# Kernel tuning notes

Measured on AMD Instinct MI355X. Metric: run time of the kernel, lower is better.

Reference implementation:

```python
import jax, jax.numpy as jnp
import numpy as np

B, L, N, C, H, COND = 2, 8, 256, 1024, 16, 64
D = C // H  # 64, divisible by 4


def setup_inputs() -> dict:
    key = jax.random.key(0)
    ks = jax.random.split(key, 16)
    w = lambda k, i, o: (jax.random.normal(k, (i, o), jnp.float32) / np.sqrt(i)).astype(jnp.float32)
    return {
        "s_frames": jax.random.normal(ks[0], (B, L, N, C), jnp.float32),
        "frame_idx": jnp.arange(L, dtype=jnp.int32),
        "seq_idx": jnp.sort(jax.random.randint(ks[1], (B, N), 0, 1024), axis=-1).astype(jnp.int32),
        "mask": jax.random.randint(ks[2], (B, L, N), 0, 2).astype(jnp.int32),
        "cond": jax.random.normal(ks[3], (B, COND), jnp.float32),
        "W_ada": w(ks[4], COND, 2 * C), "b_ada": jnp.zeros((2 * C,), jnp.float32),
        "Wq": w(ks[5], C, C), "bq": jnp.zeros((C,), jnp.float32),
        "Wk": w(ks[6], C, C), "bk": jnp.zeros((C,), jnp.float32),
        "Wv": w(ks[7], C, C), "bv": jnp.zeros((C,), jnp.float32),
        "Wo": w(ks[8], C, C), "bo": jnp.zeros((C,), jnp.float32),
    }


def _rope2d(x, pos_s, pos_f, inv_freq):
    # x: [B,H,T,D]; first half of D rotated by residue positions, second half by frame positions.
    half = x.shape[-1] // 2
    quarter = half // 2

    def rot(xh, pos):  # xh [B,H,T,half], pos [B,T]
        ang = pos[:, None, :, None] * inv_freq  # [B,1,T,quarter]
        c, s = jnp.cos(ang), jnp.sin(ang)
        x1, x2 = xh[..., :quarter], xh[..., quarter:]
        return jnp.concatenate([x1 * c - x2 * s, x1 * s + x2 * c], axis=-1)

    return jnp.concatenate([rot(x[..., :half], pos_s), rot(x[..., half:], pos_f)], axis=-1)


def reference(s_frames, frame_idx, seq_idx, mask, cond,
              W_ada, b_ada, Wq, bq, Wk, bk, Wv, bv, Wo, bo):
    Bx, Lx, Nx, Cx = s_frames.shape
    T = Lx * Nx
    Dh = Cx // H
    scale = Dh ** (-0.5)

    # AdaLN: LayerNorm (no affine) then conditional scale/shift from cond
    mu = s_frames.mean(-1, keepdims=True)
    var = ((s_frames - mu) ** 2).mean(-1, keepdims=True)
    xn = (s_frames - mu) * jax.lax.rsqrt(var + 1e-5)
    ss = cond @ W_ada + b_ada                      # [B, 2C]
    shift, sc = ss[:, :Cx], ss[:, Cx:]
    x = xn * (1.0 + sc[:, None, None, :]) + shift[:, None, None, :]

    xf = x.reshape(Bx, T, Cx)
    split = lambda t: t.reshape(Bx, T, H, Dh).transpose(0, 2, 1, 3)  # [B,H,T,D]
    q = split(xf @ Wq + bq)
    k = split(xf @ Wk + bk)
    v = split(xf @ Wv + bv)

    # 2D RoPE positions (token t = l*N + n)
    half = Dh // 2
    quarter = half // 2
    inv_freq = 1.0 / (10000.0 ** (jnp.arange(quarter, dtype=jnp.float32) * 2.0 / half))
    pos_s = jnp.tile(seq_idx, (1, Lx)).astype(jnp.float32)                                  # [B,T]
    pos_f = jnp.broadcast_to(jnp.repeat(frame_idx, Nx).astype(jnp.float32)[None], (Bx, T))  # [B,T]
    q = _rope2d(q, pos_s, pos_f, inv_freq)
    k = _rope2d(k, pos_s, pos_f, inv_freq)

    # additive bias: block-causal over frames + key padding mask
    fi = jnp.repeat(jnp.arange(Lx), Nx)                      # [T]
    future = fi[None, :] > fi[:, None]                       # [T,T] key frame > query frame
    bias = jnp.where(future, -jnp.inf, 0.0)[None, None]      # [1,1,T,T]
    pad = (mask.reshape(Bx, T) == 0)
    bias = jnp.where(pad[:, None, None, :], -jnp.inf, bias)  # [B,1,T,T]

    logits = jnp.einsum('bhtd,bhsd->bhts', q, k) * scale + bias
    w = jax.nn.softmax(logits, axis=-1)
    out = jnp.einsum('bhts,bhsd->bhtd', w, v)
    out = out.transpose(0, 2, 1, 3).reshape(Bx, Lx, Nx, Cx)
    return out @ Wo + bo
```

## Files before the change

### kernel.cpp

```cpp
#include <hip/hip_runtime.h>

typedef __bf16 bf16;
typedef __bf16 bf16x8 __attribute__((ext_vector_type(8)));
typedef __bf16 bf16x4 __attribute__((ext_vector_type(4)));
typedef float  f32x4  __attribute__((ext_vector_type(4)));

#define B_ 2
#define L_ 8
#define N_ 256
#define C_ 1024
#define H_ 16
#define D_ 64
#define T_ 2048
#define M_ 4096
#define COND_ 64

#define QSCALE 0.18033688011111372f

__device__ __forceinline__ void gload_lds16(const void* g, void* lds) {
  __builtin_amdgcn_global_load_lds((const __attribute__((address_space(1))) void*)g,
                                   (__attribute__((address_space(3))) void*)lds, 16, 0, 0);
}

__global__ __launch_bounds__(256) void k_ada(const float* __restrict__ cond,
                                             const float* __restrict__ W,
                                             const float* __restrict__ ba,
                                             float* __restrict__ ss) {
  int j = blockIdx.x * 256 + threadIdx.x;
  int b = j >> 11;
  int n = j & 2047;
  float s = ba[n];
  #pragma unroll
  for (int i = 0; i < COND_; ++i) s += cond[b * COND_ + i] * W[i * 2048 + n];
  ss[j] = s;
}

__global__ __launch_bounds__(256) void k_wt(const float* __restrict__ Wq,
                                            const float* __restrict__ Wk,
                                            const float* __restrict__ Wv,
                                            const float* __restrict__ Wo,
                                            bf16* __restrict__ Wt) {
  __shared__ float lds[64][65];
  int z = blockIdx.z;
  const float* W = (z == 0) ? Wq : (z == 1) ? Wk : (z == 2) ? Wv : Wo;
  int k0 = blockIdx.y * 64, n0 = blockIdx.x * 64;
  int tid = threadIdx.x;
  int r = tid >> 4, c4 = (tid & 15) * 4;
  #pragma unroll
  for (int p = 0; p < 4; ++p) {
    float4 v = *(const float4*)&W[(size_t)(k0 + p * 16 + r) * 1024 + n0 + c4];
    lds[p * 16 + r][c4] = v.x; lds[p * 16 + r][c4 + 1] = v.y;
    lds[p * 16 + r][c4 + 2] = v.z; lds[p * 16 + r][c4 + 3] = v.w;
  }
  __syncthreads();
  #pragma unroll
  for (int p = 0; p < 4; ++p) {
    int j = p * 16 + r;
    int i0 = c4;
    bf16x4 o;
    o[0] = (bf16)lds[i0][j]; o[1] = (bf16)lds[i0 + 1][j];
    o[2] = (bf16)lds[i0 + 2][j]; o[3] = (bf16)lds[i0 + 3][j];
    *(bf16x4*)&Wt[(size_t)(z * 1024 + n0 + j) * 1024 + k0 + i0] = o;
  }
}

__global__ __launch_bounds__(256) void k_ln(const float* __restrict__ x,
                                            const float* __restrict__ ss,
                                            bf16* __restrict__ xo) {
  int row = blockIdx.x;
  int b = row >> 11;
  int tid = threadIdx.x;
  float4 v = *(const float4*)&x[(size_t)row * 1024 + tid * 4];
  float s = v.x + v.y + v.z + v.w;
  float s2 = v.x * v.x + v.y * v.y + v.z * v.z + v.w * v.w;
  #pragma unroll
  for (int o = 32; o > 0; o >>= 1) { s += __shfl_down(s, o); s2 += __shfl_down(s2, o); }
  __shared__ float rs[4], rs2[4];
  int w = tid >> 6, l = tid & 63;
  if (l == 0) { rs[w] = s; rs2[w] = s2; }
  __syncthreads();
  s = rs[0] + rs[1] + rs[2] + rs[3];
  s2 = rs2[0] + rs2[1] + rs2[2] + rs2[3];
  float mu = s * (1.f / 1024.f);
  float var = s2 * (1.f / 1024.f) - mu * mu;
  float rinv = rsqrtf(var + 1e-5f);
  int c = tid * 4;
  float4 sh = *(const float4*)&ss[b * 2048 + c];
  float4 sc = *(const float4*)&ss[b * 2048 + 1024 + c];
  bf16x4 o;
  o[0] = (bf16)((v.x - mu) * rinv * (1.f + sc.x) + sh.x);
  o[1] = (bf16)((v.y - mu) * rinv * (1.f + sc.y) + sh.y);
  o[2] = (bf16)((v.z - mu) * rinv * (1.f + sc.z) + sh.z);
  o[3] = (bf16)((v.w - mu) * rinv * (1.f + sc.w) + sh.w);
  *(bf16x4*)&xo[(size_t)row * 1024 + c] = o;
}

__global__ __launch_bounds__(256) void k_gemm_qkv(const bf16* __restrict__ A,
                                                  const bf16* __restrict__ Bt,
                                                  const float* __restrict__ bq,
                                                  const float* __restrict__ bk,
                                                  const float* __restrict__ bv,
                                                  const int* __restrict__ seq_idx,
                                                  const int* __restrict__ frame_idx,
                                                  bf16* __restrict__ qkv,
                                                  bf16* __restrict__ vt) {
  __shared__ __attribute__((aligned(16))) bf16 As[3][64 * 32];
  __shared__ __attribute__((aligned(16))) bf16 Bs[3][128 * 32];
  const int K = 1024;
  int n0 = blockIdx.x * 128, m0 = blockIdx.y * 64;
  int tid = threadIdx.x;
  int w = tid >> 6, l = tid & 63, cc = l & 15, g = l >> 4;
  int wm = w >> 1, wn = w & 1;
  f32x4 acc[2][4] = {};
  int pxg = ((tid & 3) ^ ((tid >> 3) & 3)) * 8;
  const bf16* Ag = A + (size_t)(m0 + (tid >> 2)) * K + pxg;
  const bf16* Bg = Bt + (size_t)(n0 + (tid >> 2)) * K + pxg;
  int soff = w * 512;
  #define GSTAGE(buf, kt_)                                                      \
    do {                                                                        \
      gload_lds16(Ag + (kt_) * 32, &As[buf][soff]);                             \
      gload_lds16(Bg + (kt_) * 32, &Bs[buf][soff]);                             \
      gload_lds16(Bg + (kt_) * 32 + (size_t)64 * K, &Bs[buf][soff + 2048]);     \
    } while (0)
  GSTAGE(0, 0);
  GSTAGE(1, 1);
  int c0 = 0, c1 = 1, c2 = 2;
  int swz = (g ^ ((cc >> 1) & 3)) * 8;
  for (int kt = 0; kt < 32; ++kt) {
    if (kt + 2 < 32) {
      GSTAGE(c2, kt + 2);
      asm volatile("s_waitcnt vmcnt(6)" ::: "memory");
    } else if (kt + 1 < 32) {
      asm volatile("s_waitcnt vmcnt(3)" ::: "memory");
    } else {
      asm volatile("s_waitcnt vmcnt(0)" ::: "memory");
    }
    __builtin_amdgcn_s_barrier();
    asm volatile("" ::: "memory");
    bf16x8 a[2], bb[4];
    #pragma unroll
    for (int mi = 0; mi < 2; ++mi) a[mi] = *(const bf16x8*)&As[c0][(wm * 32 + mi * 16 + cc) * 32 + swz];
    #pragma unroll
    for (int ni = 0; ni < 4; ++ni) bb[ni] = *(const bf16x8*)&Bs[c0][(wn * 64 + ni * 16 + cc) * 32 + swz];
    #pragma unroll
    for (int mi = 0; mi < 2; ++mi)
      #pragma unroll
      for (int ni = 0; ni < 4; ++ni)
        acc[mi][ni] = __builtin_amdgcn_mfma_f32_16x16x32_bf16(a[mi], bb[ni], acc[mi][ni], 0, 0, 0);
    __builtin_amdgcn_s_barrier();
    asm volatile("" ::: "memory");
    int tmp = c0; c0 = c1; c1 = c2; c2 = tmp;
  }
  #undef GSTAGE
  int region = blockIdx.x >> 3;
  const float* bp = (region == 0) ? bq : (region == 1) ? bk : bv;
  int b = m0 >> 11;
  if (region < 2) {
    float* Ps = (float*)&As[0][0];
    if (tid < 64) Ps[tid] = (float)seq_idx[b * 256 + (m0 & 255) + tid];
    __syncthreads();
    float invf = exp2f(-0.8304820237218405f * (float)cc);
    float posf = (float)frame_idx[(m0 & 2047) >> 8];
    float snf, csf;
    sincosf(posf * invf, &snf, &csf);
    float scl = (region == 0) ? QSCALE : 1.0f;
    csf *= scl; snf *= scl;
    int colbase = n0 + wn * 64 + cc;
    float b0 = bp[colbase & 1023];
    float b1 = bp[(colbase + 16) & 1023];
    float b2 = bp[(colbase + 32) & 1023];
    float b3 = bp[(colbase + 48) & 1023];
    #pragma unroll
    for (int mi = 0; mi < 2; ++mi) {
      #pragma unroll
      for (int r = 0; r < 4; ++r) {
        int lr = wm * 32 + mi * 16 + g * 4 + r;
        float sns, css;
        sincosf(Ps[lr] * invf, &sns, &css);
        css *= scl; sns *= scl;
        float x0 = acc[mi][0][r] + b0;
        float x1 = acc[mi][1][r] + b1;
        float x2 = acc[mi][2][r] + b2;
        float x3 = acc[mi][3][r] + b3;
        bf16* op = qkv + (size_t)(m0 + lr) * 3072 + colbase;
        op[0]  = (bf16)(x0 * css - x1 * sns);
        op[16] = (bf16)(x0 * sns + x1 * css);
        op[32] = (bf16)(x2 * csf - x3 * snf);
        op[48] = (bf16)(x2 * snf + x3 * csf);
      }
    }
  } else {
    int h = (blockIdx.x - 16) * 2 + wn;
    int tbase = (m0 & 2047) + wm * 32;
    #pragma unroll
    for (int ni = 0; ni < 4; ++ni) {
      int d = ni * 16 + cc;
      float bias = bp[h * 64 + d];
      #pragma unroll
      for (int mi = 0; mi < 2; ++mi) {
        bf16x4 pk;
        #pragma unroll
        for (int r = 0; r < 4; ++r) pk[r] = (bf16)(acc[mi][ni][r] + bias);
        int t = tbase + mi * 16 + g * 4;
        *(bf16x4*)&vt[((size_t)(b * 16 + h) * 64 + d) * 2048 + t] = pk;
      }
    }
  }
}

__global__ __launch_bounds__(256) void k_gemm_o(const bf16* __restrict__ A,
                                                const bf16* __restrict__ Bt,
                                                const float* __restrict__ bo,
                                                float* __restrict__ out) {
  __shared__ __attribute__((aligned(16))) bf16 As[3][64 * 32];
  __shared__ __attribute__((aligned(16))) bf16 Bs[3][128 * 32];
  const int K = 1024;
  int n0 = blockIdx.x * 128, m0 = blockIdx.y * 64;
  int tid = threadIdx.x;
  int w = tid >> 6, l = tid & 63, cc = l & 15, g = l >> 4;
  int wm = w >> 1, wn = w & 1;
  f32x4 acc[2][4] = {};
  int pxg = ((tid & 3) ^ ((tid >> 3) & 3)) * 8;
  const bf16* Ag = A + (size_t)(m0 + (tid >> 2)) * K + pxg;
  const bf16* Bg = Bt + (size_t)(n0 + (tid >> 2)) * K + pxg;
  int soff = w * 512;
  #define GSTAGE(buf, kt_)                                                      \
    do {                                                                        \
      gload_lds16(Ag + (kt_) * 32, &As[buf][soff]);                             \
      gload_lds16(Bg + (kt_) * 32, &Bs[buf][soff]);                             \
      gload_lds16(Bg + (kt_) * 32 + (size_t)64 * K, &Bs[buf][soff + 2048]);     \
    } while (0)
  GSTAGE(0, 0);
  GSTAGE(1, 1);
  int c0 = 0, c1 = 1, c2 = 2;
  int swz = (g ^ ((cc >> 1) & 3)) * 8;
  for (int kt = 0; kt < 32; ++kt) {
    if (kt + 2 < 32) {
      GSTAGE(c2, kt + 2);
      asm volatile("s_waitcnt vmcnt(6)" ::: "memory");
    } else if (kt + 1 < 32) {
      asm volatile("s_waitcnt vmcnt(3)" ::: "memory");
    } else {
      asm volatile("s_waitcnt vmcnt(0)" ::: "memory");
    }
    __builtin_amdgcn_s_barrier();
    asm volatile("" ::: "memory");
    bf16x8 a[2], bb[4];
    #pragma unroll
    for (int mi = 0; mi < 2; ++mi) a[mi] = *(const bf16x8*)&As[c0][(wm * 32 + mi * 16 + cc) * 32 + swz];
    #pragma unroll
    for (int ni = 0; ni < 4; ++ni) bb[ni] = *(const bf16x8*)&Bs[c0][(wn * 64 + ni * 16 + cc) * 32 + swz];
    #pragma unroll
    for (int mi = 0; mi < 2; ++mi)
      #pragma unroll
      for (int ni = 0; ni < 4; ++ni)
        acc[mi][ni] = __builtin_amdgcn_mfma_f32_16x16x32_bf16(a[mi], bb[ni], acc[mi][ni], 0, 0, 0);
    __builtin_amdgcn_s_barrier();
    asm volatile("" ::: "memory");
    int tmp = c0; c0 = c1; c1 = c2; c2 = tmp;
  }
  #undef GSTAGE
  #pragma unroll
  for (int ni = 0; ni < 4; ++ni) {
    int col = n0 + wn * 64 + ni * 16 + cc;
    float bias = bo[col];
    #pragma unroll
    for (int mi = 0; mi < 2; ++mi)
      #pragma unroll
      for (int r = 0; r < 4; ++r) {
        int row = m0 + wm * 32 + mi * 16 + g * 4 + r;
        out[(size_t)row * 1024 + col] = acc[mi][ni][r] + bias;
      }
  }
}

__global__ __launch_bounds__(256) void k_attn(const bf16* __restrict__ qkv,
                                              const bf16* __restrict__ vt,
                                              const int* __restrict__ mask,
                                              bf16* __restrict__ out) {
  __shared__ __attribute__((aligned(16))) bf16 Ks[2][64 * 64];
  __shared__ __attribute__((aligned(16))) bf16 Vs[2][64 * 64];
  __shared__ __attribute__((aligned(16))) bf16 Plds[4][16][72];
  __shared__ int Ms[2048];
  int wid = blockIdx.x;
  int f = 7 - (wid >> 7);
  int rem = wid & 127;
  int h = rem >> 3;
  int b = (rem >> 2) & 1;
  int tile = rem & 3;
  int t0 = f * 256 + tile * 64;
  int nchunk = (f + 1) * 4;
  int tid = threadIdx.x;
  int w = tid >> 6, l = tid & 63, cc = l & 15, g = l >> 4;

  int rbase = w * 16 + (l >> 3);
  int px = (l & 7) ^ (l >> 3);
  int ldst = w * 1024 + l * 8;

  int trow = t0 + w * 16 + cc;
  const bf16* qp = qkv + (size_t)((size_t)b * T_ + trow) * 3072 + h * 64;
  bf16x8 aq0 = *(const bf16x8*)(qp + g * 8);
  bf16x8 aq1 = *(const bf16x8*)(qp + 32 + g * 8);
  f32x4 o[4] = {};
  f32x4 o1 = {0.f, 0.f, 0.f, 0.f};
  float mrow[4] = {-1e30f, -1e30f, -1e30f, -1e30f};
  const int* mp = mask + b * T_;

  bf16x8 onesv;
  #pragma unroll
  for (int u = 0; u < 8; ++u) onesv[u] = (bf16)1.0f;

  #pragma unroll
  for (int j = 0; j < 2; ++j)
    gload_lds16(mp + w * 512 + j * 256 + l * 4, &Ms[w * 512 + j * 256 + l * 4]);

  #define STAGE(buf, s0_)                                                              \
    do {                                                                               \
      _Pragma("unroll")                                                                \
      for (int j = 0; j < 2; ++j) {                                                    \
        int r_ = rbase + j * 8;                                                        \
        gload_lds16(qkv + (size_t)((size_t)b * T_ + (s0_) + r_) * 3072 + 1024 + h * 64 + px * 8, \
                    &Ks[buf][ldst + j * 512]);                                         \
        gload_lds16(vt + (size_t)((size_t)(b * H_ + h) * 64 + r_) * T_ + (s0_) + px * 8, \
                    &Vs[buf][ldst + j * 512]);                                         \
      }                                                                                \
    } while (0)

  STAGE(0, 0);
  int sw1 = (g ^ (cc & 7)) * 8;
  int sw2 = ((g + 4) ^ (cc & 7)) * 8;
  for (int scn = 0; scn < nchunk; ++scn) {
    int s0 = scn * 64;
    int cur = scn & 1;
    if (scn + 1 < nchunk) {
      STAGE(cur ^ 1, s0 + 64);
      asm volatile("s_waitcnt vmcnt(4)" ::: "memory");
    } else {
      asm volatile("s_waitcnt vmcnt(0)" ::: "memory");
    }
    __builtin_amdgcn_s_barrier();
    asm volatile("" ::: "memory");
    float biasv[4];
    #pragma unroll
    for (int ni = 0; ni < 4; ++ni) biasv[ni] = Ms[s0 + ni * 16 + cc] ? 0.f : -1e30f;
    f32x4 sac[4];
    #pragma unroll
    for (int ni = 0; ni < 4; ++ni) {
      int r = ni * 16 + cc;
      bf16x8 b0 = *(const bf16x8*)&Ks[cur][r * 64 + sw1];
      bf16x8 b1 = *(const bf16x8*)&Ks[cur][r * 64 + sw2];
      f32x4 z = {0.f, 0.f, 0.f, 0.f};
      sac[ni] = __builtin_amdgcn_mfma_f32_16x16x32_bf16(aq0, b0, z, 0, 0, 0);
      sac[ni] = __builtin_amdgcn_mfma_f32_16x16x32_bf16(aq1, b1, sac[ni], 0, 0, 0);
      #pragma unroll
      for (int r4 = 0; r4 < 4; ++r4) sac[ni][r4] += biasv[ni];
    }
    float pmax[4];
    #pragma unroll
    for (int r = 0; r < 4; ++r)
      pmax[r] = fmaxf(fmaxf(sac[0][r], sac[1][r]), fmaxf(sac[2][r], sac[3][r]));
    float over = fmaxf(fmaxf(pmax[0] - mrow[0], pmax[1] - mrow[1]),
                       fmaxf(pmax[2] - mrow[2], pmax[3] - mrow[3]));
    if (__any(over > 8.0f)) {
      float alpha[4];
      #pragma unroll
      for (int r = 0; r < 4; ++r) {
        float mx = pmax[r];
        mx = fmaxf(mx, __shfl_xor(mx, 1));
        mx = fmaxf(mx, __shfl_xor(mx, 2));
        mx = fmaxf(mx, __shfl_xor(mx, 4));
        mx = fmaxf(mx, __shfl_xor(mx, 8));
        float mn = fmaxf(mrow[r], mx);
        alpha[r] = exp2f(mrow[r] - mn);
        mrow[r] = mn;
      }
      #pragma unroll
      for (int ni = 0; ni < 4; ++ni)
        #pragma unroll
        for (int r = 0; r < 4; ++r)
          o[ni][r] *= alpha[r];
      #pragma unroll
      for (int r = 0; r < 4; ++r) o1[r] *= alpha[r];
    }
    #pragma unroll
    for (int ni = 0; ni < 4; ++ni)
      #pragma unroll
      for (int r = 0; r < 4; ++r)
        sac[ni][r] = exp2f(sac[ni][r] - mrow[r]);
    #pragma unroll
    for (int ni = 0; ni < 4; ++ni)
      #pragma unroll
      for (int r = 0; r < 4; ++r)
        Plds[w][g * 4 + r][cc + ni * 16] = (bf16)sac[ni][r];
    asm volatile("s_waitcnt lgkmcnt(0)" ::: "memory");
    bf16x8 ap0 = *(const bf16x8*)&Plds[w][cc][g * 8];
    bf16x8 ap1 = *(const bf16x8*)&Plds[w][cc][32 + g * 8];
    #pragma unroll
    for (int ni = 0; ni < 4; ++ni) {
      int d = ni * 16 + cc;
      bf16x8 v0 = *(const bf16x8*)&Vs[cur][d * 64 + sw1];
      bf16x8 v1 = *(const bf16x8*)&Vs[cur][d * 64 + sw2];
      o[ni] = __builtin_amdgcn_mfma_f32_16x16x32_bf16(ap0, v0, o[ni], 0, 0, 0);
      o[ni] = __builtin_amdgcn_mfma_f32_16x16x32_bf16(ap1, v1, o[ni], 0, 0, 0);
    }
    o1 = __builtin_amdgcn_mfma_f32_16x16x32_bf16(ap0, onesv, o1, 0, 0, 0);
    o1 = __builtin_amdgcn_mfma_f32_16x16x32_bf16(ap1, onesv, o1, 0, 0, 0);
    __builtin_amdgcn_s_barrier();
    asm volatile("" ::: "memory");
  }
  float rl[4];
  #pragma unroll
  for (int r = 0; r < 4; ++r) rl[r] = 1.0f / o1[r];
  #pragma unroll
  for (int ni = 0; ni < 4; ++ni)
    #pragma unroll
    for (int r = 0; r < 4; ++r) {
      int t = t0 + w * 16 + g * 4 + r;
      out[(size_t)((size_t)b * T_ + t) * 1024 + h * 64 + ni * 16 + cc] = (bf16)(o[ni][r] * rl[r]);
    }
  #undef STAGE
}

extern "C" void kernel_launch(void* const* d_in, const int* in_sizes, int n_in,
                              void* d_out, int out_size, void* d_ws, size_t ws_size,
                              hipStream_t stream) {
  const float* s_frames = (const float*)d_in[0];
  const int* frame_idx  = (const int*)d_in[1];
  const int* seq_idx    = (const int*)d_in[2];
  const int* mask       = (const int*)d_in[3];
  const float* cond     = (const float*)d_in[4];
  const float* W_ada    = (const float*)d_in[5];
  const float* b_ada    = (const float*)d_in[6];
  const float* Wq       = (const float*)d_in[7];
  const float* bq       = (const float*)d_in[8];
  const float* Wk       = (const float*)d_in[9];
  const float* bk       = (const float*)d_in[10];
  const float* Wv       = (const float*)d_in[11];
  const float* bv       = (const float*)d_in[12];
  const float* Wo       = (const float*)d_in[13];
  const float* bo       = (const float*)d_in[14];
  float* out = (float*)d_out;

  char* ws = (char*)d_ws;
  float* ss = (float*)(ws);
  bf16* xb  = (bf16*)(ws + 16384);
  bf16* Wt  = (bf16*)(ws + 16384 + 8388608);
  bf16* qkv = (bf16*)(ws + 16384 + 2 * 8388608);
  bf16* vt  = (bf16*)(ws + 16384 + 2 * 8388608 + 25165824);
  bf16* att = (bf16*)(ws + 16384 + 3 * 8388608 + 25165824);

  k_ada<<<16, 256, 0, stream>>>(cond, W_ada, b_ada, ss);
  k_wt<<<dim3(16, 16, 4), 256, 0, stream>>>(Wq, Wk, Wv, Wo, Wt);
  k_ln<<<4096, 256, 0, stream>>>(s_frames, ss, xb);
  k_gemm_qkv<<<dim3(24, 64), 256, 0, stream>>>(xb, Wt, bq, bk, bv, seq_idx, frame_idx, qkv, vt);
  k_attn<<<1024, 256, 0, stream>>>(qkv, vt, mask, att);
  k_gemm_o<<<dim3(8, 64), 256, 0, stream>>>(att, Wt + (size_t)3072 * 1024, bo, out);
}
```

Measured before the change: 143.7 us.

## Compute transposed S=K·Q^T so softmax probs feed PV MFMA from registers

The QK^T MFMA now swaps operands to produce S transposed, and the K tile uses a new swizzle and row permutation. With that layout each lane's accumulator values can be packed straight into the A operand of the PV MFMA, which removes the per-warp P staging buffer in LDS and its lgkmcnt wait. Row-max reduction becomes a two-step cross-group shuffle, and the rescale factor is broadcast with __shfl. The mask is read as int4 vectors. The risk is in the index math of the permuted K rows, swizzle and mask layout, where a mismatch would silently give wrong results.

New measurement: 134.5 us. 6.4% less time.

```diff
diff --git a/kernel.cpp b/kernel.cpp
--- a/kernel.cpp
+++ b/kernel.cpp
@@ -280,7 +280,6 @@
                                               bf16* __restrict__ out) {
   __shared__ __attribute__((aligned(16))) bf16 Ks[2][64 * 64];
   __shared__ __attribute__((aligned(16))) bf16 Vs[2][64 * 64];
-  __shared__ __attribute__((aligned(16))) bf16 Plds[4][16][72];
   __shared__ int Ms[2048];
   int wid = blockIdx.x;
   int f = 7 - (wid >> 7);
@@ -294,7 +293,8 @@
   int w = tid >> 6, l = tid & 63, cc = l & 15, g = l >> 4;
 
   int rbase = w * 16 + (l >> 3);
-  int px = (l & 7) ^ (l >> 3);
+  int pxk = (l & 7) ^ ((l >> 3) & 3);
+  int pxv = (l & 7) ^ (l >> 3);
   int ldst = w * 1024 + l * 8;
 
   int trow = t0 + w * 16 + cc;
@@ -303,7 +303,7 @@
   bf16x8 aq1 = *(const bf16x8*)(qp + 32 + g * 8);
   f32x4 o[4] = {};
   f32x4 o1 = {0.f, 0.f, 0.f, 0.f};
-  float mrow[4] = {-1e30f, -1e30f, -1e30f, -1e30f};
+  float m_p = -1e30f;
   const int* mp = mask + b * T_;
 
   bf16x8 onesv;
@@ -319,9 +319,9 @@
       _Pragma("unroll")                                                                \
       for (int j = 0; j < 2; ++j) {                                                    \
         int r_ = rbase + j * 8;                                                        \
-        gload_lds16(qkv + (size_t)((size_t)b * T_ + (s0_) + r_) * 3072 + 1024 + h * 64 + px * 8, \
+        gload_lds16(qkv + (size_t)((size_t)b * T_ + (s0_) + r_) * 3072 + 1024 + h * 64 + ((pxk ^ (j << 2)) << 3), \
                     &Ks[buf][ldst + j * 512]);                                         \
-        gload_lds16(vt + (size_t)((size_t)(b * H_ + h) * 64 + r_) * T_ + (s0_) + px * 8, \
+        gload_lds16(vt + (size_t)((size_t)(b * H_ + h) * 64 + r_) * T_ + (s0_) + (pxv << 3), \
                     &Vs[buf][ldst + j * 512]);                                         \
       }                                                                                \
     } while (0)
@@ -329,6 +329,11 @@
   STAGE(0, 0);
   int sw1 = (g ^ (cc & 7)) * 8;
   int sw2 = ((g + 4) ^ (cc & 7)) * 8;
+  int pik = (cc & 3) | (((cc >> 2) & 1) << 2);
+  int swk1 = (g ^ pik) * 8;
+  int swk2 = ((g + 4) ^ pik) * 8;
+  int rkbase = ((cc >> 2) << 3) | (cc & 3);
+
   for (int scn = 0; scn < nchunk; ++scn) {
     int s0 = scn * 64;
     int cur = scn & 1;
@@ -340,61 +345,58 @@
     }
     __builtin_amdgcn_s_barrier();
     asm volatile("" ::: "memory");
-    float biasv[4];
-    #pragma unroll
-    for (int ni = 0; ni < 4; ++ni) biasv[ni] = Ms[s0 + ni * 16 + cc] ? 0.f : -1e30f;
+
     f32x4 sac[4];
     #pragma unroll
     for (int ni = 0; ni < 4; ++ni) {
-      int r = ni * 16 + cc;
-      bf16x8 b0 = *(const bf16x8*)&Ks[cur][r * 64 + sw1];
-      bf16x8 b1 = *(const bf16x8*)&Ks[cur][r * 64 + sw2];
+      int rk = rkbase + ((ni & 1) << 2) + ((ni >> 1) << 5);
+      bf16x8 k0 = *(const bf16x8*)&Ks[cur][rk * 64 + swk1];
+      bf16x8 k1 = *(const bf16x8*)&Ks[cur][rk * 64 + swk2];
       f32x4 z = {0.f, 0.f, 0.f, 0.f};
-      sac[ni] = __builtin_amdgcn_mfma_f32_16x16x32_bf16(aq0, b0, z, 0, 0, 0);
-      sac[ni] = __builtin_amdgcn_mfma_f32_16x16x32_bf16(aq1, b1, sac[ni], 0, 0, 0);
-      #pragma unroll
-      for (int r4 = 0; r4 < 4; ++r4) sac[ni][r4] += biasv[ni];
-    }
-    float pmax[4];
-    #pragma unroll
-    for (int r = 0; r < 4; ++r)
-      pmax[r] = fmaxf(fmaxf(sac[0][r], sac[1][r]), fmaxf(sac[2][r], sac[3][r]));
-    float over = fmaxf(fmaxf(pmax[0] - mrow[0], pmax[1] - mrow[1]),
-                       fmaxf(pmax[2] - mrow[2], pmax[3] - mrow[3]));
-    if (__any(over > 8.0f)) {
-      float alpha[4];
+      sac[ni] = __builtin_amdgcn_mfma_f32_16x16x32_bf16(k0, aq0, z, 0, 0, 0);
+      sac[ni] = __builtin_amdgcn_mfma_f32_16x16x32_bf16(k1, aq1, sac[ni], 0, 0, 0);
+    }
+    #pragma unroll
+    for (int ni = 0; ni < 4; ++ni) {
+      const int4 mi = *(const int4*)&Ms[s0 + ((ni >> 1) << 5) + (g << 3) + ((ni & 1) << 2)];
+      sac[ni][0] += mi.x ? 0.f : -1e30f;
+      sac[ni][1] += mi.y ? 0.f : -1e30f;
+      sac[ni][2] += mi.z ? 0.f : -1e30f;
+      sac[ni][3] += mi.w ? 0.f : -1e30f;
+    }
+
+    float pmax = sac[0][0];
+    #pragma unroll
+    for (int ni = 0; ni < 4; ++ni)
+      #pragma unroll
+      for (int r = 0; r < 4; ++r) pmax = fmaxf(pmax, sac[ni][r]);
+    if (__any(pmax - m_p > 8.0f)) {
+      float mx = pmax;
+      mx = fmaxf(mx, __shfl_xor(mx, 16));
+      mx = fmaxf(mx, __shfl_xor(mx, 32));
+      float mn = fmaxf(m_p, mx);
+      float alpha_p = exp2f(m_p - mn);
+      m_p = mn;
       #pragma unroll
       for (int r = 0; r < 4; ++r) {
-        float mx = pmax[r];
-        mx = fmaxf(mx, __shfl_xor(mx, 1));
-        mx = fmaxf(mx, __shfl_xor(mx, 2));
-        mx = fmaxf(mx, __shfl_xor(mx, 4));
-        mx = fmaxf(mx, __shfl_xor(mx, 8));
-        float mn = fmaxf(mrow[r], mx);
-        alpha[r] = exp2f(mrow[r] - mn);
-        mrow[r] = mn;
+        float ao = __shfl(alpha_p, 4 * g + r);
+        #pragma unroll
+        for (int ni = 0; ni < 4; ++ni) o[ni][r] *= ao;
+        o1[r] *= ao;
       }
-      #pragma unroll
-      for (int ni = 0; ni < 4; ++ni)
-        #pragma unroll
-        for (int r = 0; r < 4; ++r)
-          o[ni][r] *= alpha[r];
-      #pragma unroll
-      for (int r = 0; r < 4; ++r) o1[r] *= alpha[r];
     }
     #pragma unroll
     for (int ni = 0; ni < 4; ++ni)
       #pragma unroll
       for (int r = 0; r < 4; ++r)
-        sac[ni][r] = exp2f(sac[ni][r] - mrow[r]);
-    #pragma unroll
-    for (int ni = 0; ni < 4; ++ni)
-      #pragma unroll
-      for (int r = 0; r < 4; ++r)
-        Plds[w][g * 4 + r][cc + ni * 16] = (bf16)sac[ni][r];
-    asm volatile("s_waitcnt lgkmcnt(0)" ::: "memory");
-    bf16x8 ap0 = *(const bf16x8*)&Plds[w][cc][g * 8];
-    bf16x8 ap1 = *(const bf16x8*)&Plds[w][cc][32 + g * 8];
+        sac[ni][r] = exp2f(sac[ni][r] - m_p);
+    bf16x8 ap0, ap1;
+    #pragma unroll
+    for (int j = 0; j < 4; ++j) {
+      ap0[j] = (bf16)sac[0][j]; ap0[4 + j] = (bf16)sac[1][j];
+      ap1[j] = (bf16)sac[2][j]; ap1[4 + j] = (bf16)sac[3][j];
+    }
+
     #pragma unroll
     for (int ni = 0; ni < 4; ++ni) {
       int d = ni * 16 + cc;
@@ -405,6 +407,7 @@
     }
     o1 = __builtin_amdgcn_mfma_f32_16x16x32_bf16(ap0, onesv, o1, 0, 0, 0);
     o1 = __builtin_amdgcn_mfma_f32_16x16x32_bf16(ap1, onesv, o1, 0, 0, 0);
+
     __builtin_amdgcn_s_barrier();
     asm volatile("" ::: "memory");
   }
```
